# Kernel tuning notes

Hardware: AMD Instinct MI355X
Metric: run time of the kernel (lower is better)

Reference implementation:

```python
import jax, jax.numpy as jnp
import numpy as np

N_NODES = 10000
N_EDGES = 640000
F_IN = 128
F_HID = 128
BN_EPS = 1e-5


def _spectral_norm_weight(W, u):
    # One power iteration, matching torch.nn.utils.spectral_norm defaults.
    v = W.T @ u
    v = v / (jnp.linalg.norm(v) + 1e-12)
    u_new = W @ v
    u_new = u_new / (jnp.linalg.norm(u_new) + 1e-12)
    sigma = u_new @ (W @ v)
    return W / sigma


def setup_inputs() -> dict:
    key = jax.random.key(0)
    ks = jax.random.split(key, 8)
    x = jax.random.normal(ks[0], (N_NODES, F_IN), dtype=jnp.float32)
    edge_index = jax.random.randint(ks[1], (2, N_EDGES), 0, N_NODES, dtype=jnp.int64)
    W1 = jax.random.normal(ks[2], (F_HID, F_IN), dtype=jnp.float32) * (1.0 / np.sqrt(F_IN))
    b1 = jax.random.normal(ks[3], (F_HID,), dtype=jnp.float32) * 0.01
    u1 = jax.random.normal(ks[4], (F_HID,), dtype=jnp.float32)
    gamma = jnp.ones((F_HID,), dtype=jnp.float32)
    beta = jnp.zeros((F_HID,), dtype=jnp.float32)
    W2 = jax.random.normal(ks[5], (F_HID, F_HID), dtype=jnp.float32) * (1.0 / np.sqrt(F_HID))
    b2 = jax.random.normal(ks[6], (F_HID,), dtype=jnp.float32) * 0.01
    u2 = jax.random.normal(ks[7], (F_HID,), dtype=jnp.float32)
    return {"x": x, "edge_index": edge_index, "W1": W1, "b1": b1, "u1": u1,
            "gamma": gamma, "beta": beta, "W2": W2, "b2": b2, "u2": u2}


def reference(x, edge_index, W1, b1, u1, gamma, beta, W2, b2, u2):
    src, dst = edge_index[0], edge_index[1]
    # GINConv sum aggregation: out_i = sum_{j in N(i)} x_j
    agg = jax.ops.segment_sum(x[src], dst, num_segments=N_NODES)
    h = x + agg  # eps = 0 (default, train_eps=False)
    # MLP: SN-Linear -> ReLU -> BatchNorm1d (training stats) -> SN-Linear
    h = h @ _spectral_norm_weight(W1, u1).T + b1
    h = jax.nn.relu(h)
    mu = jnp.mean(h, axis=0)
    var = jnp.mean((h - mu) ** 2, axis=0)  # biased var, as torch BN forward
    h = gamma * (h - mu) / jnp.sqrt(var + BN_EPS) + beta
    h = h @ _spectral_norm_weight(W2, u2).T + b2
    return h
```

## Files before the change

### kernel.cpp

```cpp
#include <hip/hip_runtime.h>

#define NF 128
#define FB 128
#define CB 64
#define MAXNODE 10240

__device__ __forceinline__ unsigned short f2bf(float f) {
    unsigned int u = __float_as_uint(f);
    unsigned int r = u + 0x7FFFu + ((u >> 16) & 1u);
    return (unsigned short)(r >> 16);
}

__global__ __launch_bounds__(512) void power_hist_kernel(
    const float* __restrict__ W1, const float* __restrict__ u1,
    const float* __restrict__ W2, const float* __restrict__ u2,
    const int* __restrict__ dst, int n_edges,
    int* __restrict__ hist2d, int nbin,
    const float* __restrict__ x, unsigned short* __restrict__ xb, int n_x4,
    float* __restrict__ inv_sigma, float* __restrict__ W1t,
    float* __restrict__ colzero) {
    __shared__ float Wl[128][129];
    __shared__ float us[128], vv[128], part[4][128], red[128];
    __shared__ int hist[MAXNODE];
    int tid = threadIdx.x;

    if (blockIdx.x >= 2 + FB) {
        int cb = blockIdx.x - 2 - FB;
        const float4* x4 = (const float4*)x;
        ushort4* xb4 = (ushort4*)xb;
        for (int i = cb * 512 + tid; i < n_x4; i += CB * 512) {
            float4 v = x4[i];
            ushort4 o;
            o.x = f2bf(v.x); o.y = f2bf(v.y); o.z = f2bf(v.z); o.w = f2bf(v.w);
            xb4[i] = o;
        }
        return;
    }
    if (blockIdx.x >= 2) {
        int fb = blockIdx.x - 2;
        for (int i = tid; i < nbin; i += 512) hist[i] = 0;
        __syncthreads();
        int chunk = (n_edges + FB - 1) / FB;
        int e0 = fb * chunk, e1 = min(e0 + chunk, n_edges);
        int a0 = min(e1, (e0 + 3) & ~3);
        for (int e = e0 + tid; e < a0; e += 512) atomicAdd(&hist[dst[e]], 1);
        const int4* d4 = (const int4*)dst;
        int vs = a0 >> 2, ve = e1 >> 2;
        for (int i = vs + tid; i < ve; i += 512) {
            int4 d = d4[i];
            atomicAdd(&hist[d.x], 1);
            atomicAdd(&hist[d.y], 1);
            atomicAdd(&hist[d.z], 1);
            atomicAdd(&hist[d.w], 1);
        }
        for (int e = (ve << 2) + tid; e < e1; e += 512)
            if (e >= a0) atomicAdd(&hist[dst[e]], 1);
        __syncthreads();
        for (int i = tid; i < nbin; i += 512) hist2d[(size_t)fb * nbin + i] = hist[i];
        return;
    }

    const float* W = blockIdx.x ? W2 : W1;
    const float* u = blockIdx.x ? u2 : u1;
    const float4* W4 = (const float4*)W;
    for (int j = tid; j < 4096; j += 512) {
        float4 w = W4[j];
        int r = j >> 5, c0 = (j & 31) << 2;
        Wl[r][c0] = w.x; Wl[r][c0 + 1] = w.y; Wl[r][c0 + 2] = w.z; Wl[r][c0 + 3] = w.w;
    }
    if (tid < 128) us[tid] = u[tid];
    if (blockIdx.x == 0 && tid >= 256 && tid < 512) colzero[tid - 256] = 0.f;
    __syncthreads();

    int c = tid & 127, sl = tid >> 7;
    float acc = 0.f;
#pragma unroll
    for (int j = 0; j < 32; ++j) acc = fmaf(Wl[sl * 32 + j][c], us[sl * 32 + j], acc);
    part[sl][c] = acc;
    __syncthreads();
    if (tid < 128) {
        float v = part[0][tid] + part[1][tid] + part[2][tid] + part[3][tid];
        vv[tid] = v;
        red[tid] = v * v;
    }
    __syncthreads();
    for (int s = 64; s > 0; s >>= 1) { if (tid < s) red[tid] += red[tid + s]; __syncthreads(); }
    float nv = sqrtf(red[0]) + 1e-12f;
    __syncthreads();
    if (tid < 128) vv[tid] = vv[tid] / nv;
    __syncthreads();

    float t = 0.f;
#pragma unroll
    for (int k = 0; k < 32; ++k) t = fmaf(Wl[c][sl * 32 + k], vv[sl * 32 + k], t);
    part[sl][c] = t;
    __syncthreads();
    if (tid < 128) {
        float tv = part[0][tid] + part[1][tid] + part[2][tid] + part[3][tid];
        red[tid] = tv * tv;
    }
    __syncthreads();
    for (int s = 64; s > 0; s >>= 1) { if (tid < s) red[tid] += red[tid + s]; __syncthreads(); }
    float tt = red[0];
    float is = (sqrtf(tt) + 1e-12f) / tt;
    if (tid == 0) inv_sigma[blockIdx.x] = is;
    if (blockIdx.x == 0) {
        for (int idx = tid; idx < 16384; idx += 512) {
            int k = idx >> 7, j = idx & 127;
            W1t[idx] = Wl[j][k] * is;
        }
    }
}

__global__ void scanA_kernel(int* __restrict__ hist2d, int* __restrict__ binOff, int nbin) {
    int bin = blockIdx.x * 1024 + threadIdx.x;
    if (bin >= nbin) return;
    int run = 0;
#pragma unroll 4
    for (int fb = 0; fb < FB; ++fb) {
        int v = hist2d[(size_t)fb * nbin + bin];
        hist2d[(size_t)fb * nbin + bin] = run;
        run += v;
    }
    binOff[bin] = run;
}

__global__ __launch_bounds__(1024) void scanB_kernel(int* __restrict__ binOff, int nbin) {
    __shared__ int wsum[16], wexcl[16];
    __shared__ int carry_s;
    int tid = threadIdx.x, lane = tid & 63, wv = tid >> 6;
    if (tid == 0) carry_s = 0;
    __syncthreads();
    int nr = (nbin + 1023) >> 10;
    for (int r = 0; r < nr; ++r) {
        int i = (r << 10) + tid;
        int v = (i < nbin) ? binOff[i] : 0;
        int inc = v;
        for (int off = 1; off < 64; off <<= 1) {
            int t = __shfl_up(inc, off);
            if (lane >= off) inc += t;
        }
        if (lane == 63) wsum[wv] = inc;
        __syncthreads();
        if (wv == 0) {
            int s = (lane < 16) ? wsum[lane] : 0;
            int si = s;
            for (int off = 1; off < 16; off <<= 1) {
                int t = __shfl_up(si, off);
                if (lane >= off) si += t;
            }
            if (lane < 16) wexcl[lane] = si - s;
        }
        __syncthreads();
        int excl = inc - v + wexcl[wv] + carry_s;
        if (i < nbin) binOff[i] = excl;
        __syncthreads();
        if (tid == 1023) carry_s += wexcl[15] + wsum[15];
        __syncthreads();
    }
    if (threadIdx.x == 0) binOff[nbin] = carry_s;
}

__global__ __launch_bounds__(512) void fill_kernel(
    const int* __restrict__ src, const int* __restrict__ dst,
    const int* __restrict__ hist2d, const int* __restrict__ binOff,
    int* __restrict__ bucket, int nbin, int n_edges) {
    __shared__ int cur[MAXNODE];
    int tid = threadIdx.x, fb = blockIdx.x;
    for (int i = tid; i < nbin; i += 512)
        cur[i] = hist2d[(size_t)fb * nbin + i] + binOff[i];
    __syncthreads();
    int chunk = (n_edges + FB - 1) / FB;
    int e0 = fb * chunk, e1 = min(e0 + chunk, n_edges);
    int a0 = min(e1, (e0 + 3) & ~3);
    for (int e = e0 + tid; e < a0; e += 512) {
        int pos = atomicAdd(&cur[dst[e]], 1);
        bucket[pos] = src[e];
    }
    const int4* d4 = (const int4*)dst;
    const int4* s4 = (const int4*)src;
    int vs = a0 >> 2, ve = e1 >> 2;
    for (int i = vs + tid; i < ve; i += 512) {
        int4 d = d4[i];
        int4 s = s4[i];
        int p0 = atomicAdd(&cur[d.x], 1);
        int p1 = atomicAdd(&cur[d.y], 1);
        int p2 = atomicAdd(&cur[d.z], 1);
        int p3 = atomicAdd(&cur[d.w], 1);
        bucket[p0] = s.x; bucket[p1] = s.y; bucket[p2] = s.z; bucket[p3] = s.w;
    }
    for (int e = (ve << 2) + tid; e < e1; e += 512)
        if (e >= a0) {
            int pos = atomicAdd(&cur[dst[e]], 1);
            bucket[pos] = src[e];
        }
}

__global__ __launch_bounds__(256) void gather_kernel(
    const unsigned short* __restrict__ xb, const int* __restrict__ bucket,
    const int* __restrict__ binOff, float* __restrict__ h0, int n_nodes) {
    int gw = (blockIdx.x * blockDim.x + threadIdx.x) >> 6;
    int lane = threadIdx.x & 63;
    if (gw >= n_nodes) return;
    const unsigned int* xu = (const unsigned int*)xb;
    unsigned int u0 = xu[(size_t)gw * 64 + lane];
    float2 acc;
    acc.x = __uint_as_float(u0 << 16);
    acc.y = __uint_as_float(u0 & 0xFFFF0000u);
    int j = binOff[gw], end = binOff[gw + 1];
    for (; j + 8 <= end; j += 8) {
        int s0 = bucket[j],     s1 = bucket[j + 1], s2 = bucket[j + 2], s3 = bucket[j + 3];
        int s4 = bucket[j + 4], s5 = bucket[j + 5], s6 = bucket[j + 6], s7 = bucket[j + 7];
        unsigned int v0 = xu[(size_t)s0 * 64 + lane];
        unsigned int v1 = xu[(size_t)s1 * 64 + lane];
        unsigned int v2 = xu[(size_t)s2 * 64 + lane];
        unsigned int v3 = xu[(size_t)s3 * 64 + lane];
        unsigned int v4 = xu[(size_t)s4 * 64 + lane];
        unsigned int v5 = xu[(size_t)s5 * 64 + lane];
        unsigned int v6 = xu[(size_t)s6 * 64 + lane];
        unsigned int v7 = xu[(size_t)s7 * 64 + lane];
        acc.x += __uint_as_float(v0 << 16) + __uint_as_float(v1 << 16)
               + __uint_as_float(v2 << 16) + __uint_as_float(v3 << 16)
               + __uint_as_float(v4 << 16) + __uint_as_float(v5 << 16)
               + __uint_as_float(v6 << 16) + __uint_as_float(v7 << 16);
        acc.y += __uint_as_float(v0 & 0xFFFF0000u) + __uint_as_float(v1 & 0xFFFF0000u)
               + __uint_as_float(v2 & 0xFFFF0000u) + __uint_as_float(v3 & 0xFFFF0000u)
               + __uint_as_float(v4 & 0xFFFF0000u) + __uint_as_float(v5 & 0xFFFF0000u)
               + __uint_as_float(v6 & 0xFFFF0000u) + __uint_as_float(v7 & 0xFFFF0000u);
    }
    for (; j < end; ++j) {
        unsigned int v = xu[(size_t)bucket[j] * 64 + lane];
        acc.x += __uint_as_float(v << 16);
        acc.y += __uint_as_float(v & 0xFFFF0000u);
    }
    ((float2*)h0)[(size_t)gw * 64 + lane] = acc;
}

__global__ void edge_scatter_kernel(const int* __restrict__ ei, const float* __restrict__ x,
                                    float* __restrict__ h0, int n_edges) {
    int gtid = blockIdx.x * blockDim.x + threadIdx.x;
    int wid = gtid >> 6;
    int lane = threadIdx.x & 63;
    int nw = (gridDim.x * blockDim.x) >> 6;
    const int* srcs = ei;
    const int* dsts = ei + n_edges;
    for (int e = wid; e < n_edges; e += nw) {
        int s = srcs[e];
        int d = dsts[e];
        atomicAdd(&h0[d * NF + lane], x[s * NF + lane]);
        atomicAdd(&h0[d * NF + 64 + lane], x[s * NF + 64 + lane]);
    }
}

template <bool RELU, bool BNACC>
__global__ __launch_bounds__(256, 4) void gemm_kernel(
    const float* __restrict__ H, const float* __restrict__ Wt,
    const float* __restrict__ bias, float* __restrict__ O,
    float* __restrict__ colsum, float* __restrict__ colsumsq, int n_rows) {
    __shared__ float Hl[64][128];
    int tid = threadIdx.x;
    int m0 = blockIdx.x * 64;

    const float4* H4 = (const float4*)H;
    for (int j = tid; j < 2048; j += 256) {
        int r = j >> 5, k4 = j & 31;
        int gr = m0 + r;
        float4 h = (gr < n_rows) ? H4[(size_t)gr * 32 + k4] : make_float4(0.f, 0.f, 0.f, 0.f);
        *(float4*)&Hl[r][k4 << 2] = h;
    }
    __syncthreads();

    int tx = tid & 31, ty = tid >> 5;
    int rb = ty * 8, cb = tx * 4;
    float acc[8][4] = {};
    const float4* Wt4 = (const float4*)Wt;

#pragma unroll 2
    for (int k = 0; k < 128; k += 4) {
        float4 w0 = Wt4[(k + 0) * 32 + tx];
        float4 w1 = Wt4[(k + 1) * 32 + tx];
        float4 w2 = Wt4[(k + 2) * 32 + tx];
        float4 w3 = Wt4[(k + 3) * 32 + tx];
        float wv[4][4] = {{w0.x, w0.y, w0.z, w0.w}, {w1.x, w1.y, w1.z, w1.w},
                          {w2.x, w2.y, w2.z, w2.w}, {w3.x, w3.y, w3.z, w3.w}};
#pragma unroll
        for (int i = 0; i < 8; ++i) {
            float4 h = *(const float4*)&Hl[rb + i][k];
            float hf[4] = {h.x, h.y, h.z, h.w};
#pragma unroll
            for (int kk = 0; kk < 4; ++kk)
#pragma unroll
                for (int j = 0; j < 4; ++j)
                    acc[i][j] = fmaf(hf[kk], wv[kk][j], acc[i][j]);
        }
    }

    float bv[4];
#pragma unroll
    for (int j = 0; j < 4; ++j) bv[j] = bias[cb + j];

    float s[4] = {0.f, 0.f, 0.f, 0.f}, q[4] = {0.f, 0.f, 0.f, 0.f};
#pragma unroll
    for (int i = 0; i < 8; ++i) {
        int gr = m0 + rb + i;
        if (gr < n_rows) {
            float o[4];
#pragma unroll
            for (int j = 0; j < 4; ++j) {
                float v = acc[i][j] + bv[j];
                if (RELU) v = fmaxf(v, 0.f);
                o[j] = v;
                if (BNACC) { s[j] += v; q[j] = fmaf(v, v, q[j]); }
            }
            *(float4*)&O[(size_t)gr * NF + cb] = make_float4(o[0], o[1], o[2], o[3]);
        }
    }

    if (BNACC) {
        __syncthreads();
        float* sS = &Hl[0][0];
        float* sQ = &Hl[16][0];
#pragma unroll
        for (int j = 0; j < 4; ++j) {
            sS[ty * 128 + cb + j] = s[j];
            sQ[ty * 128 + cb + j] = q[j];
        }
        __syncthreads();
        if (tid < 128) {
            float ts = 0.f, tq = 0.f;
#pragma unroll
            for (int g = 0; g < 8; ++g) {
                ts += sS[g * 128 + tid];
                tq += sQ[g * 128 + tid];
            }
            atomicAdd(&colsum[tid], ts);
            atomicAdd(&colsumsq[tid], tq);
        }
    }
}

__global__ void fold_kernel(const float* __restrict__ W2, const float* __restrict__ b2,
                            const float* __restrict__ gamma, const float* __restrict__ beta,
                            const float* __restrict__ colsum, const float* __restrict__ colsumsq,
                            const float* __restrict__ inv_sigma, float* __restrict__ W2pt,
                            float* __restrict__ b2p, float inv_n) {
    __shared__ float a[128], cc[128], red[128];
    int k = threadIdx.x;
    int j = blockIdx.x;
    float mu = colsum[k] * inv_n;
    float var = colsumsq[k] * inv_n - mu * mu;
    float ai = gamma[k] / sqrtf(var + 1e-5f);
    a[k] = ai;
    cc[k] = beta[k] - ai * mu;
    __syncthreads();
    float is2 = inv_sigma[1];
    float wv = W2[j * 128 + k] * is2;
    W2pt[k * 128 + j] = wv * a[k];
    red[k] = wv * cc[k];
    __syncthreads();
    for (int s = 64; s > 0; s >>= 1) { if (k < s) red[k] += red[k + s]; __syncthreads(); }
    if (k == 0) b2p[j] = b2[j] + red[0];
}

extern "C" void kernel_launch(void* const* d_in, const int* in_sizes, int n_in,
                              void* d_out, int out_size, void* d_ws, size_t ws_size,
                              hipStream_t stream) {
    const float* x     = (const float*)d_in[0];
    const int*   ei    = (const int*)d_in[1];
    const float* W1    = (const float*)d_in[2];
    const float* b1    = (const float*)d_in[3];
    const float* u1    = (const float*)d_in[4];
    const float* gamma = (const float*)d_in[5];
    const float* beta  = (const float*)d_in[6];
    const float* W2    = (const float*)d_in[7];
    const float* b2    = (const float*)d_in[8];
    const float* u2    = (const float*)d_in[9];
    float* out = (float*)d_out;

    int n_nodes = in_sizes[0] / NF;
    int n_edges = in_sizes[1] / 2;
    int nbin = n_nodes;
    int nbin_pad = (nbin + 1 + 3) & ~3;
    int nedge_pad = (n_edges + 3) & ~3;

    float* ws        = (float*)d_ws;
    float* inv_sigma = ws;
    float* colsum    = ws + 4;
    float* colsumsq  = colsum + 128;
    float* W1t       = colsumsq + 128;
    float* W2pt      = W1t + 16384;
    float* b2p       = W2pt + 16384;
    int*   binOff    = (int*)(b2p + 128);
    int*   bucket    = binOff + nbin_pad;
    float* h0        = (float*)(bucket + nedge_pad);
    unsigned short* xb = (unsigned short*)(h0 + (size_t)n_nodes * NF);
    int*   hist2d    = (int*)h0;

    size_t need = (size_t)(33156 + nbin_pad + nedge_pad) * 4
                + (size_t)n_nodes * NF * 4 + (size_t)n_nodes * NF * 2;
    bool fused = (n_nodes <= MAXNODE) && (ws_size >= need)
               && ((size_t)FB * nbin <= (size_t)n_nodes * NF);

    int n_x4 = n_nodes * 32;

    if (fused) {
        power_hist_kernel<<<2 + FB + CB, 512, 0, stream>>>(
            W1, u1, W2, u2, ei + n_edges, n_edges, hist2d, nbin,
            x, xb, n_x4, inv_sigma, W1t, colsum);
        scanA_kernel<<<(nbin + 1023) / 1024, 1024, 0, stream>>>(hist2d, binOff, nbin);
        scanB_kernel<<<1, 1024, 0, stream>>>(binOff, nbin);
        fill_kernel<<<FB, 512, 0, stream>>>(ei, ei + n_edges, hist2d, binOff, bucket,
                                            nbin, n_edges);
        gather_kernel<<<(n_nodes * 64 + 255) / 256, 256, 0, stream>>>(
            xb, bucket, binOff, h0, n_nodes);
    } else {
        power_hist_kernel<<<2, 512, 0, stream>>>(
            W1, u1, W2, u2, ei + n_edges, n_edges, nullptr, nbin,
            x, xb, 0, inv_sigma, W1t, colsum);
        hipMemcpyAsync(h0, x, (size_t)n_nodes * NF * sizeof(float),
                       hipMemcpyDeviceToDevice, stream);
        edge_scatter_kernel<<<2048, 256, 0, stream>>>(ei, x, h0, n_edges);
    }

    int gemm_blocks = (n_nodes + 63) / 64;

    gemm_kernel<true, true><<<gemm_blocks, 256, 0, stream>>>(
        h0, W1t, b1, out, colsum, colsumsq, n_nodes);

    fold_kernel<<<128, 128, 0, stream>>>(W2, b2, gamma, beta, colsum, colsumsq,
                                         inv_sigma, W2pt, b2p, 1.0f / (float)n_nodes);

    gemm_kernel<false, false><<<gemm_blocks, 256, 0, stream>>>(
        out, W2pt, b2p, out, nullptr, nullptr, n_nodes);
}
```

Before: 112.8 us.

## Fuse gather aggregation into first GEMM and fold BN via last-block pattern

Merges the CSR gather into the first GEMM kernel so aggregated rows stay in shared memory instead of round-tripping through a global h0 buffer. The BN fold into W2 now runs in the last block to finish, found with an atomic counter, and the two scan kernels are merged the same way. This cuts several kernel launches and one full-size global write and read. In exchange each fused block does gather and GEMM serially, the fold runs on one block, and the new counters have to be reset every call.

```diff
diff --git a/kernel.cpp b/kernel.cpp
--- a/kernel.cpp
+++ b/kernel.cpp
@@ -18,7 +18,7 @@
     int* __restrict__ hist2d, int nbin,
     const float* __restrict__ x, unsigned short* __restrict__ xb, int n_x4,
     float* __restrict__ inv_sigma, float* __restrict__ W1t,
-    float* __restrict__ colzero) {
+    float* __restrict__ colzero, int* __restrict__ cnts) {
     __shared__ float Wl[128][129];
     __shared__ float us[128], vv[128], part[4][128], red[128];
     __shared__ int hist[MAXNODE];
@@ -70,6 +70,7 @@
     }
     if (tid < 128) us[tid] = u[tid];
     if (blockIdx.x == 0 && tid >= 256 && tid < 512) colzero[tid - 256] = 0.f;
+    if (blockIdx.x == 0 && tid < 2) cnts[tid] = 0;
     __syncthreads();
 
     int c = tid & 127, sl = tid >> 7;
@@ -112,23 +113,32 @@
     }
 }
 
-__global__ void scanA_kernel(int* __restrict__ hist2d, int* __restrict__ binOff, int nbin) {
-    int bin = blockIdx.x * 1024 + threadIdx.x;
-    if (bin >= nbin) return;
-    int run = 0;
+__global__ __launch_bounds__(1024) void scanAB_kernel(int* __restrict__ hist2d,
+                                                      int* __restrict__ binOff,
+                                                      int nbin, int* __restrict__ cnt) {
+    int tid = threadIdx.x;
+    int bin = blockIdx.x * 1024 + tid;
+    if (bin < nbin) {
+        int run = 0;
 #pragma unroll 4
-    for (int fb = 0; fb < FB; ++fb) {
-        int v = hist2d[(size_t)fb * nbin + bin];
-        hist2d[(size_t)fb * nbin + bin] = run;
-        run += v;
-    }
-    binOff[bin] = run;
-}
-
-__global__ __launch_bounds__(1024) void scanB_kernel(int* __restrict__ binOff, int nbin) {
+        for (int fb = 0; fb < FB; ++fb) {
+            int v = hist2d[(size_t)fb * nbin + bin];
+            hist2d[(size_t)fb * nbin + bin] = run;
+            run += v;
+        }
+        binOff[bin] = run;
+    }
+    __threadfence();
+    __syncthreads();
+    __shared__ int isLast;
+    if (tid == 0) isLast = (atomicAdd(cnt, 1) == (int)gridDim.x - 1);
+    __syncthreads();
+    if (!isLast) return;
+    __threadfence();
+
     __shared__ int wsum[16], wexcl[16];
     __shared__ int carry_s;
-    int tid = threadIdx.x, lane = tid & 63, wv = tid >> 6;
+    int lane = tid & 63, wv = tid >> 6;
     if (tid == 0) carry_s = 0;
     __syncthreads();
     int nr = (nbin + 1023) >> 10;
@@ -158,7 +168,7 @@
         if (tid == 1023) carry_s += wexcl[15] + wsum[15];
         __syncthreads();
     }
-    if (threadIdx.x == 0) binOff[nbin] = carry_s;
+    if (tid == 0) binOff[nbin] = carry_s;
 }
 
 __global__ __launch_bounds__(512) void fill_kernel(
@@ -196,44 +206,157 @@
         }
 }
 
-__global__ __launch_bounds__(256) void gather_kernel(
+__global__ __launch_bounds__(512, 2) void agg_gemm1_kernel(
     const unsigned short* __restrict__ xb, const int* __restrict__ bucket,
-    const int* __restrict__ binOff, float* __restrict__ h0, int n_nodes) {
-    int gw = (blockIdx.x * blockDim.x + threadIdx.x) >> 6;
-    int lane = threadIdx.x & 63;
-    if (gw >= n_nodes) return;
+    const int* __restrict__ binOff, const float* __restrict__ W1t,
+    const float* __restrict__ b1, float* __restrict__ O,
+    float* __restrict__ colsum, float* __restrict__ colsumsq,
+    const float* __restrict__ W2, const float* __restrict__ b2,
+    const float* __restrict__ gamma, const float* __restrict__ beta,
+    const float* __restrict__ inv_sigma, float* __restrict__ W2pt,
+    float* __restrict__ b2p, int* __restrict__ cnt,
+    int n_nodes, float inv_n) {
+    __shared__ float Hl[64][128];
+    int tid = threadIdx.x;
+    int m0 = blockIdx.x * 64;
+    int lane = tid & 63, w = tid >> 6;
     const unsigned int* xu = (const unsigned int*)xb;
-    unsigned int u0 = xu[(size_t)gw * 64 + lane];
-    float2 acc;
-    acc.x = __uint_as_float(u0 << 16);
-    acc.y = __uint_as_float(u0 & 0xFFFF0000u);
-    int j = binOff[gw], end = binOff[gw + 1];
-    for (; j + 8 <= end; j += 8) {
-        int s0 = bucket[j],     s1 = bucket[j + 1], s2 = bucket[j + 2], s3 = bucket[j + 3];
-        int s4 = bucket[j + 4], s5 = bucket[j + 5], s6 = bucket[j + 6], s7 = bucket[j + 7];
-        unsigned int v0 = xu[(size_t)s0 * 64 + lane];
-        unsigned int v1 = xu[(size_t)s1 * 64 + lane];
-        unsigned int v2 = xu[(size_t)s2 * 64 + lane];
-        unsigned int v3 = xu[(size_t)s3 * 64 + lane];
-        unsigned int v4 = xu[(size_t)s4 * 64 + lane];
-        unsigned int v5 = xu[(size_t)s5 * 64 + lane];
-        unsigned int v6 = xu[(size_t)s6 * 64 + lane];
-        unsigned int v7 = xu[(size_t)s7 * 64 + lane];
-        acc.x += __uint_as_float(v0 << 16) + __uint_as_float(v1 << 16)
-               + __uint_as_float(v2 << 16) + __uint_as_float(v3 << 16)
-               + __uint_as_float(v4 << 16) + __uint_as_float(v5 << 16)
-               + __uint_as_float(v6 << 16) + __uint_as_float(v7 << 16);
-        acc.y += __uint_as_float(v0 & 0xFFFF0000u) + __uint_as_float(v1 & 0xFFFF0000u)
-               + __uint_as_float(v2 & 0xFFFF0000u) + __uint_as_float(v3 & 0xFFFF0000u)
-               + __uint_as_float(v4 & 0xFFFF0000u) + __uint_as_float(v5 & 0xFFFF0000u)
-               + __uint_as_float(v6 & 0xFFFF0000u) + __uint_as_float(v7 & 0xFFFF0000u);
-    }
-    for (; j < end; ++j) {
-        unsigned int v = xu[(size_t)bucket[j] * 64 + lane];
-        acc.x += __uint_as_float(v << 16);
-        acc.y += __uint_as_float(v & 0xFFFF0000u);
-    }
-    ((float2*)h0)[(size_t)gw * 64 + lane] = acc;
+
+    for (int nrel = w; nrel < 64; nrel += 8) {
+        int gn = m0 + nrel;
+        float2 acc = make_float2(0.f, 0.f);
+        if (gn < n_nodes) {
+            unsigned int u0 = xu[(size_t)gn * 64 + lane];
+            acc.x = __uint_as_float(u0 << 16);
+            acc.y = __uint_as_float(u0 & 0xFFFF0000u);
+            int j = binOff[gn], end = binOff[gn + 1];
+            for (; j + 8 <= end; j += 8) {
+                int s0 = bucket[j],     s1 = bucket[j + 1], s2 = bucket[j + 2], s3 = bucket[j + 3];
+                int s4 = bucket[j + 4], s5 = bucket[j + 5], s6 = bucket[j + 6], s7 = bucket[j + 7];
+                unsigned int v0 = xu[(size_t)s0 * 64 + lane];
+                unsigned int v1 = xu[(size_t)s1 * 64 + lane];
+                unsigned int v2 = xu[(size_t)s2 * 64 + lane];
+                unsigned int v3 = xu[(size_t)s3 * 64 + lane];
+                unsigned int v4 = xu[(size_t)s4 * 64 + lane];
+                unsigned int v5 = xu[(size_t)s5 * 64 + lane];
+                unsigned int v6 = xu[(size_t)s6 * 64 + lane];
+                unsigned int v7 = xu[(size_t)s7 * 64 + lane];
+                acc.x += __uint_as_float(v0 << 16) + __uint_as_float(v1 << 16)
+                       + __uint_as_float(v2 << 16) + __uint_as_float(v3 << 16)
+                       + __uint_as_float(v4 << 16) + __uint_as_float(v5 << 16)
+                       + __uint_as_float(v6 << 16) + __uint_as_float(v7 << 16);
+                acc.y += __uint_as_float(v0 & 0xFFFF0000u) + __uint_as_float(v1 & 0xFFFF0000u)
+                       + __uint_as_float(v2 & 0xFFFF0000u) + __uint_as_float(v3 & 0xFFFF0000u)
+                       + __uint_as_float(v4 & 0xFFFF0000u) + __uint_as_float(v5 & 0xFFFF0000u)
+                       + __uint_as_float(v6 & 0xFFFF0000u) + __uint_as_float(v7 & 0xFFFF0000u);
+            }
+            for (; j < end; ++j) {
+                unsigned int v = xu[(size_t)bucket[j] * 64 + lane];
+                acc.x += __uint_as_float(v << 16);
+                acc.y += __uint_as_float(v & 0xFFFF0000u);
+            }
+        }
+        Hl[nrel][lane * 2] = acc.x;
+        Hl[nrel][lane * 2 + 1] = acc.y;
+    }
+    __syncthreads();
+
+    int tx = tid & 31, ty = tid >> 5;
+    int rb = ty * 4, cb = tx * 4;
+    float acc4[4][4] = {};
+    const float4* Wt4 = (const float4*)W1t;
+#pragma unroll 2
+    for (int k = 0; k < 128; k += 4) {
+        float4 w0 = Wt4[(k + 0) * 32 + tx];
+        float4 w1 = Wt4[(k + 1) * 32 + tx];
+        float4 w2 = Wt4[(k + 2) * 32 + tx];
+        float4 w3 = Wt4[(k + 3) * 32 + tx];
+        float wv[4][4] = {{w0.x, w0.y, w0.z, w0.w}, {w1.x, w1.y, w1.z, w1.w},
+                          {w2.x, w2.y, w2.z, w2.w}, {w3.x, w3.y, w3.z, w3.w}};
+#pragma unroll
+        for (int i = 0; i < 4; ++i) {
+            float4 h = *(const float4*)&Hl[rb + i][k];
+            float hf[4] = {h.x, h.y, h.z, h.w};
+#pragma unroll
+            for (int kk = 0; kk < 4; ++kk)
+#pragma unroll
+                for (int jj = 0; jj < 4; ++jj)
+                    acc4[i][jj] = fmaf(hf[kk], wv[kk][jj], acc4[i][jj]);
+        }
+    }
+
+    float bv[4];
+#pragma unroll
+    for (int jj = 0; jj < 4; ++jj) bv[jj] = b1[cb + jj];
+
+    float s[4] = {0.f, 0.f, 0.f, 0.f}, q[4] = {0.f, 0.f, 0.f, 0.f};
+#pragma unroll
+    for (int i = 0; i < 4; ++i) {
+        int gr = m0 + rb + i;
+        if (gr < n_nodes) {
+            float o[4];
+#pragma unroll
+            for (int jj = 0; jj < 4; ++jj) {
+                float v = acc4[i][jj] + bv[jj];
+                v = fmaxf(v, 0.f);
+                o[jj] = v;
+                s[jj] += v;
+                q[jj] = fmaf(v, v, q[jj]);
+            }
+            *(float4*)&O[(size_t)gr * NF + cb] = make_float4(o[0], o[1], o[2], o[3]);
+        }
+    }
+
+    __syncthreads();
+    float* sS = &Hl[0][0];
+    float* sQ = &Hl[0][0] + 2048;
+#pragma unroll
+    for (int jj = 0; jj < 4; ++jj) {
+        sS[ty * 128 + cb + jj] = s[jj];
+        sQ[ty * 128 + cb + jj] = q[jj];
+    }
+    __syncthreads();
+    if (tid < 128) {
+        float ts = 0.f, tq = 0.f;
+#pragma unroll
+        for (int g = 0; g < 16; ++g) {
+            ts += sS[g * 128 + tid];
+            tq += sQ[g * 128 + tid];
+        }
+        atomicAdd(&colsum[tid], ts);
+        atomicAdd(&colsumsq[tid], tq);
+    }
+
+    __threadfence();
+    __syncthreads();
+    __shared__ int isLast;
+    if (tid == 0) isLast = (atomicAdd(cnt, 1) == (int)gridDim.x - 1);
+    __syncthreads();
+    if (!isLast) return;
+    __threadfence();
+
+    __shared__ float a_s[128], c_s[128], bred[512];
+    if (tid < 128) {
+        float mu = colsum[tid] * inv_n;
+        float var = colsumsq[tid] * inv_n - mu * mu;
+        float ai = gamma[tid] / sqrtf(var + 1e-5f);
+        a_s[tid] = ai;
+        c_s[tid] = beta[tid] - ai * mu;
+    }
+    __syncthreads();
+    float is2 = inv_sigma[1];
+    int j = tid & 127, quarter = tid >> 7;
+    int k0 = quarter * 32;
+    float bacc = 0.f;
+    for (int k = k0; k < k0 + 32; ++k) {
+        float wvv = W2[j * 128 + k] * is2;
+        W2pt[k * 128 + j] = wvv * a_s[k];
+        bacc = fmaf(wvv, c_s[k], bacc);
+    }
+    bred[tid] = bacc;
+    __syncthreads();
+    if (tid < 128)
+        b2p[tid] = b2[tid] + bred[tid] + bred[tid + 128] + bred[tid + 256] + bred[tid + 384];
 }
 
 __global__ void edge_scatter_kernel(const int* __restrict__ ei, const float* __restrict__ x,
@@ -382,6 +505,9 @@
     int nbin = n_nodes;
     int nbin_pad = (nbin + 1 + 3) & ~3;
     int nedge_pad = (n_edges + 3) & ~3;
+    size_t scratch = (size_t)FB * nbin > (size_t)n_nodes * NF
+                   ? (size_t)FB * nbin : (size_t)n_nodes * NF;
+    scratch = (scratch + 3) & ~(size_t)3;
 
     float* ws        = (float*)d_ws;
     float* inv_sigma = ws;
@@ -390,45 +516,45 @@
     float* W1t       = colsumsq + 128;
     float* W2pt      = W1t + 16384;
     float* b2p       = W2pt + 16384;
-    int*   binOff    = (int*)(b2p + 128);
+    int*   cnts      = (int*)(b2p + 128);
+    int*   binOff    = cnts + 4;
     int*   bucket    = binOff + nbin_pad;
-    float* h0        = (float*)(bucket + nedge_pad);
-    unsigned short* xb = (unsigned short*)(h0 + (size_t)n_nodes * NF);
-    int*   hist2d    = (int*)h0;
-
-    size_t need = (size_t)(33156 + nbin_pad + nedge_pad) * 4
-                + (size_t)n_nodes * NF * 4 + (size_t)n_nodes * NF * 2;
-    bool fused = (n_nodes <= MAXNODE) && (ws_size >= need)
-               && ((size_t)FB * nbin <= (size_t)n_nodes * NF);
+    int*   hist2d    = bucket + nedge_pad;
+    float* h0        = (float*)hist2d;
+    unsigned short* xb = (unsigned short*)(hist2d + scratch);
+
+    size_t need = (size_t)(33160 + nbin_pad + nedge_pad + scratch) * 4
+                + (size_t)n_nodes * NF * 2;
+    bool fused = (n_nodes <= MAXNODE) && (ws_size >= need);
 
     int n_x4 = n_nodes * 32;
+    int gemm_blocks = (n_nodes + 63) / 64;
 
     if (fused) {
         power_hist_kernel<<<2 + FB + CB, 512, 0, stream>>>(
             W1, u1, W2, u2, ei + n_edges, n_edges, hist2d, nbin,
-            x, xb, n_x4, inv_sigma, W1t, colsum);
-        scanA_kernel<<<(nbin + 1023) / 1024, 1024, 0, stream>>>(hist2d, binOff, nbin);
-        scanB_kernel<<<1, 1024, 0, stream>>>(binOff, nbin);
+            x, xb, n_x4, inv_sigma, W1t, colsum, cnts);
+        scanAB_kernel<<<(nbin + 1023) / 1024, 1024, 0, stream>>>(hist2d, binOff, nbin,
+                                                                 &cnts[0]);
         fill_kernel<<<FB, 512, 0, stream>>>(ei, ei + n_edges, hist2d, binOff, bucket,
                                             nbin, n_edges);
-        gather_kernel<<<(n_nodes * 64 + 255) / 256, 256, 0, stream>>>(
-            xb, bucket, binOff, h0, n_nodes);
+        agg_gemm1_kernel<<<gemm_blocks, 512, 0, stream>>>(
+            xb, bucket, binOff, W1t, b1, out, colsum, colsumsq,
+            W2, b2, gamma, beta, inv_sigma, W2pt, b2p, &cnts[1],
+            n_nodes, 1.0f / (float)n_nodes);
     } else {
         power_hist_kernel<<<2, 512, 0, stream>>>(
-            W1, u1, W2, u2, ei + n_edges, n_edges, nullptr, nbin,
-            x, xb, 0, inv_sigma, W1t, colsum);
+            W1, u1, W2, u2, ei + n_edges, n_edges, hist2d, nbin,
+            x, xb, 0, inv_sigma, W1t, colsum, cnts);
         hipMemcpyAsync(h0, x, (size_t)n_nodes * NF * sizeof(float),
                        hipMemcpyDeviceToDevice, stream);
         edge_scatter_kernel<<<2048, 256, 0, stream>>>(ei, x, h0, n_edges);
-    }
-
-    int gemm_blocks = (n_nodes + 63) / 64;
-
-    gemm_kernel<true, true><<<gemm_blocks, 256, 0, stream>>>(
-        h0, W1t, b1, out, colsum, colsumsq, n_nodes);
-
-    fold_kernel<<<128, 128, 0, stream>>>(W2, b2, gamma, beta, colsum, colsumsq,
-                                         inv_sigma, W2pt, b2p, 1.0f / (float)n_nodes);
+        gemm_kernel<true, true><<<gemm_blocks, 256, 0, stream>>>(
+            h0, W1t, b1, out, colsum, colsumsq, n_nodes);
+        fold_kernel<<<128, 128, 0, stream>>>(W2, b2, gamma, beta, colsum, colsumsq,
+                                             inv_sigma, W2pt, b2p,
+                                             1.0f / (float)n_nodes);
+    }
 
     gemm_kernel<false, false><<<gemm_blocks, 256, 0, stream>>>(
         out, W2pt, b2p, out, nullptr, nullptr, n_nodes);
```

New measurement: 170.1 us. +50.7%, slower.

## Merge scan passes and fold BN into GEMM via last-block completion counters

Applied to the files above, without the earlier changes.

Combines the two scan kernels into one launch in which the last block to finish (detected with an atomic counter) performs the global exclusive scan. The BN-fold kernel is likewise moved into the tail of the first GEMM, run by its last-finishing block. The workspace layout is also rearranged so hist2d and h0 get separate regions. This removes two kernel launches and their inter-kernel gaps, but leaves the fold and the global scan running serially on a single block while the rest of the GPU idles.

```diff
diff --git a/kernel.cpp b/kernel.cpp
--- a/kernel.cpp
+++ b/kernel.cpp
@@ -18,7 +18,7 @@
     int* __restrict__ hist2d, int nbin,
     const float* __restrict__ x, unsigned short* __restrict__ xb, int n_x4,
     float* __restrict__ inv_sigma, float* __restrict__ W1t,
-    float* __restrict__ colzero) {
+    float* __restrict__ colzero, int* __restrict__ cnts) {
     __shared__ float Wl[128][129];
     __shared__ float us[128], vv[128], part[4][128], red[128];
     __shared__ int hist[MAXNODE];
@@ -70,6 +70,7 @@
     }
     if (tid < 128) us[tid] = u[tid];
     if (blockIdx.x == 0 && tid >= 256 && tid < 512) colzero[tid - 256] = 0.f;
+    if (blockIdx.x == 0 && tid < 2) cnts[tid] = 0;
     __syncthreads();
 
     int c = tid & 127, sl = tid >> 7;
@@ -112,23 +113,32 @@
     }
 }
 
-__global__ void scanA_kernel(int* __restrict__ hist2d, int* __restrict__ binOff, int nbin) {
-    int bin = blockIdx.x * 1024 + threadIdx.x;
-    if (bin >= nbin) return;
-    int run = 0;
+__global__ __launch_bounds__(1024) void scanAB_kernel(int* __restrict__ hist2d,
+                                                      int* __restrict__ binOff,
+                                                      int nbin, int* __restrict__ cnt) {
+    int tid = threadIdx.x;
+    int bin = blockIdx.x * 1024 + tid;
+    if (bin < nbin) {
+        int run = 0;
 #pragma unroll 4
-    for (int fb = 0; fb < FB; ++fb) {
-        int v = hist2d[(size_t)fb * nbin + bin];
-        hist2d[(size_t)fb * nbin + bin] = run;
-        run += v;
-    }
-    binOff[bin] = run;
-}
-
-__global__ __launch_bounds__(1024) void scanB_kernel(int* __restrict__ binOff, int nbin) {
+        for (int fb = 0; fb < FB; ++fb) {
+            int v = hist2d[(size_t)fb * nbin + bin];
+            hist2d[(size_t)fb * nbin + bin] = run;
+            run += v;
+        }
+        binOff[bin] = run;
+    }
+    __threadfence();
+    __syncthreads();
+    __shared__ int isLast;
+    if (tid == 0) isLast = (atomicAdd(cnt, 1) == (int)gridDim.x - 1);
+    __syncthreads();
+    if (!isLast) return;
+    __threadfence();
+
     __shared__ int wsum[16], wexcl[16];
     __shared__ int carry_s;
-    int tid = threadIdx.x, lane = tid & 63, wv = tid >> 6;
+    int lane = tid & 63, wv = tid >> 6;
     if (tid == 0) carry_s = 0;
     __syncthreads();
     int nr = (nbin + 1023) >> 10;
@@ -158,7 +168,7 @@
         if (tid == 1023) carry_s += wexcl[15] + wsum[15];
         __syncthreads();
     }
-    if (threadIdx.x == 0) binOff[nbin] = carry_s;
+    if (tid == 0) binOff[nbin] = carry_s;
 }
 
 __global__ __launch_bounds__(512) void fill_kernel(
@@ -252,11 +262,15 @@
     }
 }
 
-template <bool RELU, bool BNACC>
+template <bool RELU, bool BNACC, bool FOLD>
 __global__ __launch_bounds__(256, 4) void gemm_kernel(
     const float* __restrict__ H, const float* __restrict__ Wt,
     const float* __restrict__ bias, float* __restrict__ O,
-    float* __restrict__ colsum, float* __restrict__ colsumsq, int n_rows) {
+    float* __restrict__ colsum, float* __restrict__ colsumsq, int n_rows,
+    const float* __restrict__ W2, const float* __restrict__ b2,
+    const float* __restrict__ gamma, const float* __restrict__ beta,
+    const float* __restrict__ inv_sigma, float* __restrict__ W2pt,
+    float* __restrict__ b2p, int* __restrict__ cnt, float inv_n) {
     __shared__ float Hl[64][128];
     int tid = threadIdx.x;
     int m0 = blockIdx.x * 64;
@@ -337,29 +351,38 @@
             atomicAdd(&colsumsq[tid], tq);
         }
     }
-}
-
-__global__ void fold_kernel(const float* __restrict__ W2, const float* __restrict__ b2,
-                            const float* __restrict__ gamma, const float* __restrict__ beta,
-                            const float* __restrict__ colsum, const float* __restrict__ colsumsq,
-                            const float* __restrict__ inv_sigma, float* __restrict__ W2pt,
-                            float* __restrict__ b2p, float inv_n) {
-    __shared__ float a[128], cc[128], red[128];
-    int k = threadIdx.x;
-    int j = blockIdx.x;
-    float mu = colsum[k] * inv_n;
-    float var = colsumsq[k] * inv_n - mu * mu;
-    float ai = gamma[k] / sqrtf(var + 1e-5f);
-    a[k] = ai;
-    cc[k] = beta[k] - ai * mu;
-    __syncthreads();
-    float is2 = inv_sigma[1];
-    float wv = W2[j * 128 + k] * is2;
-    W2pt[k * 128 + j] = wv * a[k];
-    red[k] = wv * cc[k];
-    __syncthreads();
-    for (int s = 64; s > 0; s >>= 1) { if (k < s) red[k] += red[k + s]; __syncthreads(); }
-    if (k == 0) b2p[j] = b2[j] + red[0];
+
+    if (FOLD) {
+        __threadfence();
+        __syncthreads();
+        __shared__ int isLast;
+        if (tid == 0) isLast = (atomicAdd(cnt, 1) == (int)gridDim.x - 1);
+        __syncthreads();
+        if (!isLast) return;
+        __threadfence();
+
+        __shared__ float a_s[128], c_s[128], bred[256];
+        if (tid < 128) {
+            float mu = colsum[tid] * inv_n;
+            float var = colsumsq[tid] * inv_n - mu * mu;
+            float ai = gamma[tid] / sqrtf(var + 1e-5f);
+            a_s[tid] = ai;
+            c_s[tid] = beta[tid] - ai * mu;
+        }
+        __syncthreads();
+        float is2 = inv_sigma[0];
+        int j = tid & 127, half = tid >> 7;
+        int k0 = half * 64;
+        float bacc = 0.f;
+        for (int k = k0; k < k0 + 64; ++k) {
+            float wvv = W2[j * 128 + k] * is2;
+            W2pt[k * 128 + j] = wvv * a_s[k];
+            bacc = fmaf(wvv, c_s[k], bacc);
+        }
+        bred[tid] = bacc;
+        __syncthreads();
+        if (tid < 128) b2p[tid] = b2[tid] + bred[tid] + bred[tid + 128];
+    }
 }
 
 extern "C" void kernel_launch(void* const* d_in, const int* in_sizes, int n_in,
@@ -382,6 +405,9 @@
     int nbin = n_nodes;
     int nbin_pad = (nbin + 1 + 3) & ~3;
     int nedge_pad = (n_edges + 3) & ~3;
+    size_t scratch = (size_t)FB * nbin > (size_t)n_nodes * NF
+                   ? (size_t)FB * nbin : (size_t)n_nodes * NF;
+    scratch = (scratch + 3) & ~(size_t)3;
 
     float* ws        = (float*)d_ws;
     float* inv_sigma = ws;
@@ -390,46 +416,50 @@
     float* W1t       = colsumsq + 128;
     float* W2pt      = W1t + 16384;
     float* b2p       = W2pt + 16384;
-    int*   binOff    = (int*)(b2p + 128);
+    int*   cnts      = (int*)(b2p + 128);
+    int*   binOff    = cnts + 4;
     int*   bucket    = binOff + nbin_pad;
-    float* h0        = (float*)(bucket + nedge_pad);
-    unsigned short* xb = (unsigned short*)(h0 + (size_t)n_nodes * NF);
-    int*   hist2d    = (int*)h0;
-
-    size_t need = (size_t)(33156 + nbin_pad + nedge_pad) * 4
-                + (size_t)n_nodes * NF * 4 + (size_t)n_nodes * NF * 2;
-    bool fused = (n_nodes <= MAXNODE) && (ws_size >= need)
-               && ((size_t)FB * nbin <= (size_t)n_nodes * NF);
+    int*   hist2d    = bucket + nedge_pad;
+    float* h0        = (float*)hist2d;
+    float* h0f       = (float*)(hist2d + scratch);
+    unsigned short* xb = (unsigned short*)(hist2d + scratch);
+    float* h0g       = (float*)(xb + (size_t)n_nodes * NF);
+
+    size_t need = (size_t)(33160 + nbin_pad + nedge_pad + scratch) * 4
+                + (size_t)n_nodes * NF * 2 + (size_t)n_nodes * NF * 4;
+    bool fused = (n_nodes <= MAXNODE) && (ws_size >= need);
 
     int n_x4 = n_nodes * 32;
+    int gemm_blocks = (n_nodes + 63) / 64;
 
     if (fused) {
         power_hist_kernel<<<2 + FB + CB, 512, 0, stream>>>(
             W1, u1, W2, u2, ei + n_edges, n_edges, hist2d, nbin,
-            x, xb, n_x4, inv_sigma, W1t, colsum);
-        scanA_kernel<<<(nbin + 1023) / 1024, 1024, 0, stream>>>(hist2d, binOff, nbin);
-        scanB_kernel<<<1, 1024, 0, stream>>>(binOff, nbin);
+            x, xb, n_x4, inv_sigma, W1t, colsum, cnts);
+        scanAB_kernel<<<(nbin + 1023) / 1024, 1024, 0, stream>>>(hist2d, binOff, nbin,
+                                                                 &cnts[0]);
         fill_kernel<<<FB, 512, 0, stream>>>(ei, ei + n_edges, hist2d, binOff, bucket,
                                             nbin, n_edges);
         gather_kernel<<<(n_nodes * 64 + 255) / 256, 256, 0, stream>>>(
-            xb, bucket, binOff, h0, n_nodes);
+            xb, bucket, binOff, h0g, n_nodes);
+        gemm_kernel<true, true, true><<<gemm_blocks, 256, 0, stream>>>(
+            h0g, W1t, b1, out, colsum, colsumsq, n_nodes,
+            W2, b2, gamma, beta, inv_sigma + 1, W2pt, b2p, &cnts[1],
+            1.0f / (float)n_nodes);
     } else {
         power_hist_kernel<<<2, 512, 0, stream>>>(
-            W1, u1, W2, u2, ei + n_edges, n_edges, nullptr, nbin,
-            x, xb, 0, inv_sigma, W1t, colsum);
+            W1, u1, W2, u2, ei + n_edges, n_edges, hist2d, nbin,
+            x, xb, 0, inv_sigma, W1t, colsum, cnts);
         hipMemcpyAsync(h0, x, (size_t)n_nodes * NF * sizeof(float),
                        hipMemcpyDeviceToDevice, stream);
         edge_scatter_kernel<<<2048, 256, 0, stream>>>(ei, x, h0, n_edges);
-    }
-
-    int gemm_blocks = (n_nodes + 63) / 64;
-
-    gemm_kernel<true, true><<<gemm_blocks, 256, 0, stream>>>(
-        h0, W1t, b1, out, colsum, colsumsq, n_nodes);
-
-    fold_kernel<<<128, 128, 0, stream>>>(W2, b2, gamma, beta, colsum, colsumsq,
-                                         inv_sigma, W2pt, b2p, 1.0f / (float)n_nodes);
-
-    gemm_kernel<false, false><<<gemm_blocks, 256, 0, stream>>>(
-        out, W2pt, b2p, out, nullptr, nullptr, n_nodes);
-}
+        gemm_kernel<true, true, true><<<gemm_blocks, 256, 0, stream>>>(
+            h0, W1t, b1, out, colsum, colsumsq, n_nodes,
+            W2, b2, gamma, beta, inv_sigma + 1, W2pt, b2p, &cnts[1],
+            1.0f / (float)n_nodes);
+    }
+
+    gemm_kernel<false, false, false><<<gemm_blocks, 256, 0, stream>>>(
+        out, W2pt, b2p, out, nullptr, nullptr, n_nodes,
+        nullptr, nullptr, nullptr, nullptr, nullptr, nullptr, nullptr, nullptr, 0.f);
+}
```

New measurement: 139.7 us. 1.24x slower.

## Merge scan kernels with last-block pattern and shrink GEMM row tiles to 16

Applied to the files above, without the earlier changes.

Merges the two-stage prefix scan into one launch: the last block to finish, detected with an atomic counter, performs the global scan. The GEMM tile drops from 64 to 16 rows per block, which quadruples the number of blocks for the 10k-row problem so more of the chip is occupied, at the cost of reloading the weights more often. The workspace layout also changes so the gathered features no longer share the histogram buffer. The goal is to remove one kernel launch and underutilisation in both GEMMs.

```diff
diff --git a/kernel.cpp b/kernel.cpp
--- a/kernel.cpp
+++ b/kernel.cpp
@@ -18,7 +18,7 @@
     int* __restrict__ hist2d, int nbin,
     const float* __restrict__ x, unsigned short* __restrict__ xb, int n_x4,
     float* __restrict__ inv_sigma, float* __restrict__ W1t,
-    float* __restrict__ colzero) {
+    float* __restrict__ colzero, int* __restrict__ cnts) {
     __shared__ float Wl[128][129];
     __shared__ float us[128], vv[128], part[4][128], red[128];
     __shared__ int hist[MAXNODE];
@@ -70,6 +70,7 @@
     }
     if (tid < 128) us[tid] = u[tid];
     if (blockIdx.x == 0 && tid >= 256 && tid < 512) colzero[tid - 256] = 0.f;
+    if (blockIdx.x == 0 && tid < 2) cnts[tid] = 0;
     __syncthreads();
 
     int c = tid & 127, sl = tid >> 7;
@@ -112,23 +113,32 @@
     }
 }
 
-__global__ void scanA_kernel(int* __restrict__ hist2d, int* __restrict__ binOff, int nbin) {
-    int bin = blockIdx.x * 1024 + threadIdx.x;
-    if (bin >= nbin) return;
-    int run = 0;
+__global__ __launch_bounds__(1024) void scanAB_kernel(int* __restrict__ hist2d,
+                                                      int* __restrict__ binOff,
+                                                      int nbin, int* __restrict__ cnt) {
+    int tid = threadIdx.x;
+    int bin = blockIdx.x * 1024 + tid;
+    if (bin < nbin) {
+        int run = 0;
 #pragma unroll 4
-    for (int fb = 0; fb < FB; ++fb) {
-        int v = hist2d[(size_t)fb * nbin + bin];
-        hist2d[(size_t)fb * nbin + bin] = run;
-        run += v;
-    }
-    binOff[bin] = run;
-}
-
-__global__ __launch_bounds__(1024) void scanB_kernel(int* __restrict__ binOff, int nbin) {
+        for (int fb = 0; fb < FB; ++fb) {
+            int v = hist2d[(size_t)fb * nbin + bin];
+            hist2d[(size_t)fb * nbin + bin] = run;
+            run += v;
+        }
+        binOff[bin] = run;
+    }
+    __threadfence();
+    __syncthreads();
+    __shared__ int isLast;
+    if (tid == 0) isLast = (atomicAdd(cnt, 1) == (int)gridDim.x - 1);
+    __syncthreads();
+    if (!isLast) return;
+    __threadfence();
+
     __shared__ int wsum[16], wexcl[16];
     __shared__ int carry_s;
-    int tid = threadIdx.x, lane = tid & 63, wv = tid >> 6;
+    int lane = tid & 63, wv = tid >> 6;
     if (tid == 0) carry_s = 0;
     __syncthreads();
     int nr = (nbin + 1023) >> 10;
@@ -158,7 +168,7 @@
         if (tid == 1023) carry_s += wexcl[15] + wsum[15];
         __syncthreads();
     }
-    if (threadIdx.x == 0) binOff[nbin] = carry_s;
+    if (tid == 0) binOff[nbin] = carry_s;
 }
 
 __global__ __launch_bounds__(512) void fill_kernel(
@@ -253,16 +263,16 @@
 }
 
 template <bool RELU, bool BNACC>
-__global__ __launch_bounds__(256, 4) void gemm_kernel(
+__global__ __launch_bounds__(256, 4) void gemm16_kernel(
     const float* __restrict__ H, const float* __restrict__ Wt,
     const float* __restrict__ bias, float* __restrict__ O,
     float* __restrict__ colsum, float* __restrict__ colsumsq, int n_rows) {
-    __shared__ float Hl[64][128];
+    __shared__ float Hl[16][128];
     int tid = threadIdx.x;
-    int m0 = blockIdx.x * 64;
+    int m0 = blockIdx.x * 16;
 
     const float4* H4 = (const float4*)H;
-    for (int j = tid; j < 2048; j += 256) {
+    for (int j = tid; j < 512; j += 256) {
         int r = j >> 5, k4 = j & 31;
         int gr = m0 + r;
         float4 h = (gr < n_rows) ? H4[(size_t)gr * 32 + k4] : make_float4(0.f, 0.f, 0.f, 0.f);
@@ -271,8 +281,8 @@
     __syncthreads();
 
     int tx = tid & 31, ty = tid >> 5;
-    int rb = ty * 8, cb = tx * 4;
-    float acc[8][4] = {};
+    int rb = ty * 2, cb = tx * 4;
+    float acc[2][4] = {};
     const float4* Wt4 = (const float4*)Wt;
 
 #pragma unroll 2
@@ -284,7 +294,7 @@
         float wv[4][4] = {{w0.x, w0.y, w0.z, w0.w}, {w1.x, w1.y, w1.z, w1.w},
                           {w2.x, w2.y, w2.z, w2.w}, {w3.x, w3.y, w3.z, w3.w}};
 #pragma unroll
-        for (int i = 0; i < 8; ++i) {
+        for (int i = 0; i < 2; ++i) {
             float4 h = *(const float4*)&Hl[rb + i][k];
             float hf[4] = {h.x, h.y, h.z, h.w};
 #pragma unroll
@@ -301,7 +311,7 @@
 
     float s[4] = {0.f, 0.f, 0.f, 0.f}, q[4] = {0.f, 0.f, 0.f, 0.f};
 #pragma unroll
-    for (int i = 0; i < 8; ++i) {
+    for (int i = 0; i < 2; ++i) {
         int gr = m0 + rb + i;
         if (gr < n_rows) {
             float o[4];
@@ -319,7 +329,7 @@
     if (BNACC) {
         __syncthreads();
         float* sS = &Hl[0][0];
-        float* sQ = &Hl[16][0];
+        float* sQ = &Hl[8][0];
 #pragma unroll
         for (int j = 0; j < 4; ++j) {
             sS[ty * 128 + cb + j] = s[j];
@@ -382,6 +392,9 @@
     int nbin = n_nodes;
     int nbin_pad = (nbin + 1 + 3) & ~3;
     int nedge_pad = (n_edges + 3) & ~3;
+    size_t scratch = (size_t)FB * nbin > (size_t)n_nodes * NF
+                   ? (size_t)FB * nbin : (size_t)n_nodes * NF;
+    scratch = (scratch + 3) & ~(size_t)3;
 
     float* ws        = (float*)d_ws;
     float* inv_sigma = ws;
@@ -390,46 +403,47 @@
     float* W1t       = colsumsq + 128;
     float* W2pt      = W1t + 16384;
     float* b2p       = W2pt + 16384;
-    int*   binOff    = (int*)(b2p + 128);
+    int*   cnts      = (int*)(b2p + 128);
+    int*   binOff    = cnts + 4;
     int*   bucket    = binOff + nbin_pad;
-    float* h0        = (float*)(bucket + nedge_pad);
-    unsigned short* xb = (unsigned short*)(h0 + (size_t)n_nodes * NF);
-    int*   hist2d    = (int*)h0;
-
-    size_t need = (size_t)(33156 + nbin_pad + nedge_pad) * 4
-                + (size_t)n_nodes * NF * 4 + (size_t)n_nodes * NF * 2;
-    bool fused = (n_nodes <= MAXNODE) && (ws_size >= need)
-               && ((size_t)FB * nbin <= (size_t)n_nodes * NF);
+    int*   hist2d    = bucket + nedge_pad;
+    float* h0        = (float*)hist2d;
+    unsigned short* xb = (unsigned short*)(hist2d + scratch);
+    float* h0g       = (float*)(xb + (size_t)n_nodes * NF);
+
+    size_t need = (size_t)(33160 + nbin_pad + nedge_pad + scratch) * 4
+                + (size_t)n_nodes * NF * 2 + (size_t)n_nodes * NF * 4;
+    bool fused = (n_nodes <= MAXNODE) && (ws_size >= need);
 
     int n_x4 = n_nodes * 32;
+    int gemm_blocks = (n_nodes + 15) / 16;
 
     if (fused) {
         power_hist_kernel<<<2 + FB + CB, 512, 0, stream>>>(
             W1, u1, W2, u2, ei + n_edges, n_edges, hist2d, nbin,
-            x, xb, n_x4, inv_sigma, W1t, colsum);
-        scanA_kernel<<<(nbin + 1023) / 1024, 1024, 0, stream>>>(hist2d, binOff, nbin);
-        scanB_kernel<<<1, 1024, 0, stream>>>(binOff, nbin);
+            x, xb, n_x4, inv_sigma, W1t, colsum, cnts);
+        scanAB_kernel<<<(nbin + 1023) / 1024, 1024, 0, stream>>>(hist2d, binOff, nbin,
+                                                                 &cnts[0]);
         fill_kernel<<<FB, 512, 0, stream>>>(ei, ei + n_edges, hist2d, binOff, bucket,
                                             nbin, n_edges);
         gather_kernel<<<(n_nodes * 64 + 255) / 256, 256, 0, stream>>>(
-            xb, bucket, binOff, h0, n_nodes);
+            xb, bucket, binOff, h0g, n_nodes);
+        gemm16_kernel<true, true><<<gemm_blocks, 256, 0, stream>>>(
+            h0g, W1t, b1, out, colsum, colsumsq, n_nodes);
     } else {
         power_hist_kernel<<<2, 512, 0, stream>>>(
-            W1, u1, W2, u2, ei + n_edges, n_edges, nullptr, nbin,
-            x, xb, 0, inv_sigma, W1t, colsum);
+            W1, u1, W2, u2, ei + n_edges, n_edges, hist2d, nbin,
+            x, xb, 0, inv_sigma, W1t, colsum, cnts);
         hipMemcpyAsync(h0, x, (size_t)n_nodes * NF * sizeof(float),
                        hipMemcpyDeviceToDevice, stream);
         edge_scatter_kernel<<<2048, 256, 0, stream>>>(ei, x, h0, n_edges);
-    }
-
-    int gemm_blocks = (n_nodes + 63) / 64;
-
-    gemm_kernel<true, true><<<gemm_blocks, 256, 0, stream>>>(
-        h0, W1t, b1, out, colsum, colsumsq, n_nodes);
+        gemm16_kernel<true, true><<<gemm_blocks, 256, 0, stream>>>(
+            h0, W1t, b1, out, colsum, colsumsq, n_nodes);
+    }
 
     fold_kernel<<<128, 128, 0, stream>>>(W2, b2, gamma, beta, colsum, colsumsq,
                                          inv_sigma, W2pt, b2p, 1.0f / (float)n_nodes);
 
-    gemm_kernel<false, false><<<gemm_blocks, 256, 0, stream>>>(
+    gemm16_kernel<false, false><<<gemm_blocks, 256, 0, stream>>>(
         out, W2pt, b2p, out, nullptr, nullptr, n_nodes);
 }
```

Result: slower. 133.8 us (+18.6%).
